# Kernel tuning notes

Measured on AMD Instinct MI355X. Metric: run time of the kernel, lower is better.

The kernel has to match this reference:

```python
import jax, jax.numpy as jnp
import numpy as np

B, T, C, H, MEM = 2, 2048, 1024, 16, 256
HD = C // H


def setup_inputs() -> dict:
    key = jax.random.key(0)
    ks = jax.random.split(key, 6)
    return {
        "x": jax.random.normal(ks[0], (B, T, C), dtype=jnp.float32),
        "ext_mem": jax.random.normal(ks[1], (B, MEM, C), dtype=jnp.float32),
        "W_attn": jax.random.normal(ks[2], (C, 3 * C), dtype=jnp.float32) * 0.02,
        "b_attn": jax.random.normal(ks[3], (3 * C,), dtype=jnp.float32) * 0.02,
        "W_proj": jax.random.normal(ks[4], (C, C), dtype=jnp.float32) * 0.02,
        "b_proj": jax.random.normal(ks[5], (C,), dtype=jnp.float32) * 0.02,
    }


def reference(x, ext_mem, W_attn, b_attn, W_proj, b_proj):
    Bx, Tx, Cx = x.shape
    qkv = x @ W_attn + b_attn                      # [B,T,3C]
    q, k, v = jnp.split(qkv, 3, axis=-1)
    # [B,H,T,HD]
    q = q.reshape(Bx, Tx, H, HD).transpose(0, 2, 1, 3)
    k = k.reshape(Bx, Tx, H, HD).transpose(0, 2, 1, 3)
    v = v.reshape(Bx, Tx, H, HD).transpose(0, 2, 1, 3)
    mem = ext_mem.reshape(Bx, -1, H, HD).transpose(0, 2, 1, 3)  # [B,H,MEM,HD]
    k = jnp.concatenate([mem, k], axis=2)          # [B,H,MEM+T,HD]
    v = jnp.concatenate([mem, v], axis=2)
    mem_len = k.shape[2] - Tx
    scale = 1.0 / jnp.sqrt(jnp.float32(HD))
    att = jnp.einsum("bhtd,bhsd->bhts", q, k) * scale  # [B,H,T,MEM+T]
    # memory prefix fully attended; causal over the T query positions
    rows = jnp.arange(Tx)[:, None]
    cols = jnp.arange(mem_len + Tx)[None, :]
    allowed = (cols < mem_len) | ((cols - mem_len) <= rows)  # [T,MEM+T]
    att = jnp.where(allowed[None, None], att, jnp.float32(-jnp.inf))
    att = jax.nn.softmax(att, axis=-1)
    y = jnp.einsum("bhts,bhsd->bhtd", att, v)      # [B,H,T,HD]
    y = y.transpose(0, 2, 1, 3).reshape(Bx, Tx, Cx)
    return y @ W_proj + b_proj
```

## Files before the change

kernel.cpp:

```cpp
#include <hip/hip_runtime.h>

#define B_    2
#define T_    2048
#define C_    1024
#define H_    16
#define HD_   64
#define MEM_  256
#define S_    2304
#define NKT_  36

typedef __attribute__((ext_vector_type(8))) short short8;
typedef __attribute__((ext_vector_type(4))) short short4v;
typedef __attribute__((ext_vector_type(4))) float f32x4;

__device__ __forceinline__ unsigned short f2bf(float x) {
    return (unsigned short)((__float_as_uint(x) + 0x8000u) >> 16);
}

__device__ __forceinline__ unsigned int pk2bf(float lo, float hi) {
    unsigned int a = __float_as_uint(lo) + 0x8000u;
    unsigned int b = __float_as_uint(hi) + 0x8000u;
    return __builtin_amdgcn_perm(b, a, 0x07060302);
}

typedef const __attribute__((address_space(1))) unsigned int* gp_t;
typedef __attribute__((address_space(3))) unsigned int* lp_t;

__device__ __forceinline__ void gll16(const unsigned short* g, unsigned short* l) {
    __builtin_amdgcn_global_load_lds((gp_t)g, (lp_t)l, 16, 0, 0);
}

#define C1_ 0.18033688011112042f

__global__ __launch_bounds__(256) void prep_all(
    const float* __restrict__ x, const float* __restrict__ Wa,
    const float* __restrict__ Wp, const float* __restrict__ ext,
    unsigned short* __restrict__ x_tl, unsigned short* __restrict__ WtA,
    unsigned short* __restrict__ WtP, unsigned short* __restrict__ k_ws,
    unsigned short* __restrict__ v_tl)
{
    __shared__ float L[64][65];
    const int bid = blockIdx.x, tid = threadIdx.x;
    if (bid < 4096) {
        int i = bid * 256 + tid;
        int c = (i & 255) * 4;
        int m = i >> 8;
        float4 v = ((const float4*)x)[i];
        ushort4 o;
        o.x = f2bf(v.x); o.y = f2bf(v.y); o.z = f2bf(v.z); o.w = f2bf(v.w);
        int mt = m >> 7, r = m & 127, kc = c >> 5, cc = c & 31;
        int p = (cc >> 3) ^ ((r >> 1) & 3);
        *(ushort4*)&x_tl[(((size_t)mt * 32 + kc) << 12) + (r << 5) + p * 8 + (cc & 7)] = o;
    } else if (bid < 5120) {
        const float* in; unsigned short* out; int Cc, r0, c0;
        if (bid < 4864) {
            int r = bid - 4096; in = Wa; out = WtA; Cc = 3 * C_;
            c0 = (r % 48) * 64; r0 = (r / 48) * 64;
        } else {
            int r = bid - 4864; in = Wp; out = WtP; Cc = C_;
            c0 = (r & 15) * 64; r0 = (r >> 4) * 64;
        }
        const int jj = tid >> 4;
        const int i4 = (tid & 15) * 4;
#pragma unroll
        for (int t = 0; t < 4; ++t) {
            int j = jj + t * 16;
            float4 v = *(const float4*)(in + (size_t)(r0 + j) * Cc + c0 + i4);
            L[i4 + 0][j] = v.x; L[i4 + 1][j] = v.y;
            L[i4 + 2][j] = v.z; L[i4 + 3][j] = v.w;
        }
        __syncthreads();
#pragma unroll
        for (int t = 0; t < 4; ++t) {
            int n = c0 + jj + t * 16;
            int k = r0 + i4;
            ushort4 o;
            o.x = f2bf(L[jj + t * 16][i4 + 0]); o.y = f2bf(L[jj + t * 16][i4 + 1]);
            o.z = f2bf(L[jj + t * 16][i4 + 2]); o.w = f2bf(L[jj + t * 16][i4 + 3]);
            int nt = n >> 7, r = n & 127, kc = k >> 5, cc = k & 31;
            int p = (cc >> 3) ^ ((r >> 1) & 3);
            *(ushort4*)&out[(((size_t)nt * 32 + kc) << 12) + (r << 5) + p * 8 + (cc & 7)] = o;
        }
    } else {
        int idx = (bid - 5120) * 256 + tid;
        float val = ext[idx];
        int c = idx & (C_ - 1), m = (idx >> 10) & (MEM_ - 1), b = idx >> 18;
        int h = c >> 6, d = c & 63;
        int bh = b * H_ + h;
        unsigned short bv = f2bf(val);
        k_ws[(size_t)bh * S_ * 64 + (size_t)m * 64 + (((d >> 3) ^ (m & 7)) << 3) + (d & 7)] = bv;
        int ts = m >> 6, key = m & 63;
        v_tl[(((size_t)bh * NKT_ + ts) * 64 + d) * 64 + (((key >> 3) ^ (d & 7)) << 3) + (key & 7)] = bv;
    }
}

__global__ __launch_bounds__(256) void qkv_gemm(
    const unsigned short* __restrict__ A,
    const unsigned short* __restrict__ Bt,
    const float* __restrict__ bias,
    unsigned short* __restrict__ q_ws,
    unsigned short* __restrict__ k_ws,
    unsigned short* __restrict__ v_tl)
{
    __shared__ __align__(16) unsigned short As[2][4096];
    __shared__ __align__(16) unsigned short Bs[2][4096];
    const int tid = threadIdx.x, lane = tid & 63, wave = tid >> 6;
    const int wr = wave >> 1, wc = wave & 1;
    const size_t abase = (size_t)blockIdx.y * 32 * 4096;
    const size_t bbase = (size_t)blockIdx.x * 32 * 4096;

    f32x4 acc[4][4];
#pragma unroll
    for (int i = 0; i < 4; ++i)
#pragma unroll
        for (int j = 0; j < 4; ++j) acc[i][j] = (f32x4){0.f, 0.f, 0.f, 0.f};

    auto stage = [&](int kc, int buf) {
        const unsigned short* ga = A + abase + (size_t)kc * 4096;
        const unsigned short* gb = Bt + bbase + (size_t)kc * 4096;
#pragma unroll
        for (int s = 0; s < 2; ++s) {
            int seg = wave + s * 4;
            gll16(ga + seg * 512 + lane * 8, &As[buf][seg * 512]);
            gll16(gb + seg * 512 + lane * 8, &Bs[buf][seg * 512]);
        }
    };

    stage(0, 0);
    __syncthreads();
    for (int kc = 0; kc < 32; ++kc) {
        if (kc + 1 < 32) stage(kc + 1, (kc + 1) & 1);
        const unsigned short* as = As[kc & 1];
        const unsigned short* bs = Bs[kc & 1];
        short8 af[4], bf4[4];
#pragma unroll
        for (int i = 0; i < 4; ++i) {
            int row = wr * 64 + i * 16 + (lane & 15);
            int ph = (lane >> 4) ^ ((row >> 1) & 3);
            af[i] = *(const short8*)&as[row * 32 + ph * 8];
        }
#pragma unroll
        for (int j = 0; j < 4; ++j) {
            int row = wc * 64 + j * 16 + (lane & 15);
            int ph = (lane >> 4) ^ ((row >> 1) & 3);
            bf4[j] = *(const short8*)&bs[row * 32 + ph * 8];
        }
#pragma unroll
        for (int i = 0; i < 4; ++i)
#pragma unroll
            for (int j = 0; j < 4; ++j)
                acc[i][j] = __builtin_amdgcn_mfma_f32_16x16x32_bf16(
                    af[i], bf4[j], acc[i][j], 0, 0, 0);
        __syncthreads();
    }

#pragma unroll
    for (int j = 0; j < 4; ++j) {
        int n = blockIdx.x * 128 + wc * 64 + j * 16 + (lane & 15);
        float bs = bias[n];
        int sel = n >> 10, h = (n >> 6) & 15, d = n & 63;
#pragma unroll
        for (int i = 0; i < 4; ++i) {
            int m = blockIdx.y * 128 + wr * 64 + i * 16 + (lane >> 4) * 4;
            int b = m >> 11, t0 = m & (T_ - 1);
            int bh = b * H_ + h;
            if (sel == 0) {
                size_t base = ((size_t)bh * T_ + t0) * 64 + d;
#pragma unroll
                for (int r = 0; r < 4; ++r)
                    q_ws[base + (size_t)r * 64] = f2bf((acc[i][j][r] + bs) * C1_);
            } else if (sel == 1) {
#pragma unroll
                for (int r = 0; r < 4; ++r) {
                    int s = MEM_ + t0 + r;
                    k_ws[(size_t)bh * S_ * 64 + (size_t)s * 64
                         + (((d >> 3) ^ (s & 7)) << 3) + (d & 7)] =
                        f2bf(acc[i][j][r] + bs);
                }
            } else {
                int s0 = MEM_ + t0, ts = s0 >> 6, key = s0 & 63;
                ushort4 pv;
                pv.x = f2bf(acc[i][j][0] + bs);
                pv.y = f2bf(acc[i][j][1] + bs);
                pv.z = f2bf(acc[i][j][2] + bs);
                pv.w = f2bf(acc[i][j][3] + bs);
                *(ushort4*)&v_tl[(((size_t)bh * NKT_ + ts) * 64 + d) * 64
                                 + (((key >> 3) ^ (d & 7)) << 3) + (key & 7)] = pv;
            }
        }
    }
}

__global__ __launch_bounds__(256) void proj_gemm(
    const unsigned short* __restrict__ A,
    const unsigned short* __restrict__ Bt,
    const float* __restrict__ bias,
    float* __restrict__ out)
{
    __shared__ __align__(16) unsigned short As[2][2048];
    __shared__ __align__(16) unsigned short Bs[2][4096];
    const int tid = threadIdx.x, lane = tid & 63, wave = tid >> 6;
    const int m64 = blockIdx.y;
    const size_t abase = ((size_t)(m64 >> 1) * 32) * 4096 + (size_t)(m64 & 1) * 2048;
    const size_t bbase = (size_t)blockIdx.x * 32 * 4096;

    f32x4 acc[4][2];
#pragma unroll
    for (int i = 0; i < 4; ++i)
#pragma unroll
        for (int j = 0; j < 2; ++j) acc[i][j] = (f32x4){0.f, 0.f, 0.f, 0.f};

    auto stage = [&](int kc, int buf) {
        const unsigned short* ga = A + abase + (size_t)kc * 4096;
        const unsigned short* gb = Bt + bbase + (size_t)kc * 4096;
        gll16(ga + wave * 512 + lane * 8, &As[buf][wave * 512]);
        gll16(gb + wave * 512 + lane * 8, &Bs[buf][wave * 512]);
        gll16(gb + (wave + 4) * 512 + lane * 8, &Bs[buf][(wave + 4) * 512]);
    };

    stage(0, 0);
    __syncthreads();
    for (int kc = 0; kc < 32; ++kc) {
        if (kc + 1 < 32) stage(kc + 1, (kc + 1) & 1);
        const unsigned short* as = As[kc & 1];
        const unsigned short* bs = Bs[kc & 1];
        short8 af[4], bf2[2];
#pragma unroll
        for (int i = 0; i < 4; ++i) {
            int row = i * 16 + (lane & 15);
            int ph = (lane >> 4) ^ ((row >> 1) & 3);
            af[i] = *(const short8*)&as[row * 32 + ph * 8];
        }
#pragma unroll
        for (int j = 0; j < 2; ++j) {
            int row = wave * 32 + j * 16 + (lane & 15);
            int ph = (lane >> 4) ^ ((row >> 1) & 3);
            bf2[j] = *(const short8*)&bs[row * 32 + ph * 8];
        }
#pragma unroll
        for (int i = 0; i < 4; ++i)
#pragma unroll
            for (int j = 0; j < 2; ++j)
                acc[i][j] = __builtin_amdgcn_mfma_f32_16x16x32_bf16(
                    af[i], bf2[j], acc[i][j], 0, 0, 0);
        __syncthreads();
    }

#pragma unroll
    for (int j = 0; j < 2; ++j) {
        int n = blockIdx.x * 128 + wave * 32 + j * 16 + (lane & 15);
        float bs = bias[n];
#pragma unroll
        for (int i = 0; i < 4; ++i) {
            int m = m64 * 64 + i * 16 + (lane >> 4) * 4;
#pragma unroll
            for (int r = 0; r < 4; ++r)
                out[(size_t)(m + r) * C_ + n] = acc[i][j][r] + bs;
        }
    }
}

__global__ __launch_bounds__(256, 4) void flash_mfma(
    const unsigned short* __restrict__ qg,
    const unsigned short* __restrict__ kg,
    const unsigned short* __restrict__ vg,
    unsigned short* __restrict__ yt)
{
    __shared__ __align__(16) unsigned short Ks[2][4096];
    __shared__ __align__(16) unsigned short Vs[2][4096];

    const int tid = threadIdx.x, lane = tid & 63, wq = tid >> 6;
    const int quad = lane >> 4;
    const int a = blockIdx.x;
    const int h = blockIdx.y, b = blockIdx.z;
    const int qt = (h & 8) ? a : (31 - a);
    const int nt = 5 + qt;
    const int bh = b * H_ + h;
    const size_t kgb = (size_t)bh * S_ * 64;
    const size_t vgb = (size_t)bh * NKT_ * 4096;

    short8 qf[2];
    {
        const unsigned short* p = qg + ((size_t)bh * T_ + qt * 64 + wq * 16
                                        + (lane & 15)) * 64 + quad * 8;
        qf[0] = *(const short8*)p; qf[1] = *(const short8*)(p + 32);
    }

    f32x4 o[4];
#pragma unroll
    for (int j = 0; j < 4; ++j) o[j] = (f32x4){0.f, 0.f, 0.f, 0.f};
    float l = 0.f;

    const unsigned short* kB0 = &Ks[0][(lane & 15) * 64 + ((quad ^ (lane & 7)) * 8)];
    const unsigned short* kB1 = &Ks[0][(lane & 15) * 64 + (((quad + 4) ^ (lane & 7)) * 8)];
    const unsigned short* vPs[4];
#pragma unroll
    for (int kb = 0; kb < 4; ++kb)
        vPs[kb] = &Vs[0][(lane & 15) * 64
                         + (((kb * 2 + (lane >> 5)) ^ (lane & 7)) * 8)
                         + (quad & 1) * 4];

    auto stageTo = [&](int kt, int ofs) {
        const unsigned short* gk = kg + kgb + (size_t)kt * 4096;
        const unsigned short* gv = vg + vgb + (size_t)kt * 4096;
        gll16(gk + wq * 512 + lane * 8, &Ks[0][ofs + wq * 512]);
        gll16(gk + (wq + 4) * 512 + lane * 8, &Ks[0][ofs + (wq + 4) * 512]);
        gll16(gv + wq * 512 + lane * 8, &Vs[0][ofs + wq * 512]);
        gll16(gv + (wq + 4) * 512 + lane * 8, &Vs[0][ofs + (wq + 4) * 512]);
    };

    const int tq = qt * 64 + wq * 16 + (lane & 15);

    stageTo(0, 0);
    stageTo(1, 4096);
    for (int kt = 0; kt < nt; ++kt) {
        const int B = (kt & 1) << 12;
        if (kt + 1 < nt) asm volatile("s_waitcnt vmcnt(4)" ::: "memory");
        else             asm volatile("s_waitcnt vmcnt(0)" ::: "memory");
        __builtin_amdgcn_s_barrier();
        __builtin_amdgcn_sched_barrier(0);
        {
            const bool diag = (kt == nt - 1);
            const int s0 = kt * 64;
            short8 kA[4][2];
#pragma unroll
            for (int kb = 0; kb < 4; ++kb) {
                kA[kb][0] = *(const short8*)&kB0[B + kb * 1024];
                kA[kb][1] = *(const short8*)&kB1[B + kb * 1024];
            }
            short4v vF[4][4];
#pragma unroll
            for (int kb = 0; kb < 4; ++kb)
#pragma unroll
                for (int dblk = 0; dblk < 4; ++dblk)
                    vF[kb][dblk] = *(const short4v*)&vPs[kb][B + dblk * 1024];

#pragma unroll
            for (int kb = 0; kb < 4; ++kb) {
                f32x4 z = (f32x4){0.f, 0.f, 0.f, 0.f};
                z = __builtin_amdgcn_mfma_f32_16x16x32_bf16(kA[kb][0], qf[0], z, 0, 0, 0);
                z = __builtin_amdgcn_mfma_f32_16x16x32_bf16(kA[kb][1], qf[1], z, 0, 0, 0);
                float p[4];
#pragma unroll
                for (int r = 0; r < 4; ++r) {
                    float e = exp2f(z[r]);
                    if (diag) {
                        int key = s0 + kb * 16 + quad * 4 + r;
                        if (key - MEM_ > tq) e = 0.f;
                    }
                    l += e;
                    p[r] = e;
                }
                unsigned int r01 = pk2bf(p[0], p[1]);
                unsigned int r23 = pk2bf(p[2], p[3]);
                short4v pf;
                *(unsigned int*)&pf = r01;
                *((unsigned int*)&pf + 1) = r23;
#pragma unroll
                for (int dblk = 0; dblk < 4; ++dblk)
                    o[dblk] = __builtin_amdgcn_mfma_f32_16x16x16bf16_1k(
                        pf, vF[kb][dblk], o[dblk], 0, 0, 0);
            }
        }
        asm volatile("s_waitcnt lgkmcnt(0)" ::: "memory");
        __builtin_amdgcn_s_barrier();
        if (kt + 2 < nt) stageTo(kt + 2, B);
    }

    l += __shfl_xor(l, 16);
    l += __shfl_xor(l, 32);
    float linv[4];
#pragma unroll
    for (int r = 0; r < 4; ++r)
        linv[r] = 1.f / __shfl(l, quad * 4 + r);
#pragma unroll
    for (int dblk = 0; dblk < 4; ++dblk) {
        int c = h * 64 + dblk * 16 + (lane & 15);
        int kc = c >> 5, cc = c & 31;
#pragma unroll
        for (int r = 0; r < 4; ++r) {
            int t = qt * 64 + wq * 16 + quad * 4 + r;
            int m = b * T_ + t;
            int mt = m >> 7, rr = m & 127;
            int p = (cc >> 3) ^ ((rr >> 1) & 3);
            yt[(((size_t)mt * 32 + kc) << 12) + (rr << 5) + p * 8 + (cc & 7)] =
                f2bf(o[dblk][r] * linv[r]);
        }
    }
}

extern "C" void kernel_launch(void* const* d_in, const int* in_sizes, int n_in,
                              void* d_out, int out_size, void* d_ws, size_t ws_size,
                              hipStream_t stream) {
    (void)in_sizes; (void)n_in; (void)out_size; (void)ws_size;
    const float* x      = (const float*)d_in[0];
    const float* ext    = (const float*)d_in[1];
    const float* W_attn = (const float*)d_in[2];
    const float* b_attn = (const float*)d_in[3];
    const float* W_proj = (const float*)d_in[4];
    const float* b_proj = (const float*)d_in[5];
    float* out = (float*)d_out;

    unsigned short* x_tl  = (unsigned short*)d_ws;
    unsigned short* WtA   = x_tl + 4194304;
    unsigned short* WtP   = WtA + 3145728;
    unsigned short* q_ws  = WtP + 1048576;
    unsigned short* k_ws  = q_ws + 4194304;
    unsigned short* v_tl  = k_ws + 4718592;
    unsigned short* y_tl  = v_tl + 4718592;

    dim3 blk(256);
    prep_all<<<7168, blk, 0, stream>>>(x, W_attn, W_proj, ext,
                                       x_tl, WtA, WtP, k_ws, v_tl);
    qkv_gemm<<<dim3(24, 32), blk, 0, stream>>>(
        x_tl, WtA, b_attn, q_ws, k_ws, v_tl);
    flash_mfma<<<dim3(32, H_, B_), blk, 0, stream>>>(q_ws, k_ws, v_tl, y_tl);
    proj_gemm<<<dim3(8, 64), blk, 0, stream>>>(y_tl, WtP, b_proj, out);
}
```

Before: 202.2 us.

## Double query tile per flash block to reuse staged K/V across two row groups

```diff
diff --git a/kernel.cpp b/kernel.cpp
--- a/kernel.cpp
+++ b/kernel.cpp
@@ -260,7 +260,7 @@
     }
 }
 
-__global__ __launch_bounds__(256, 4) void flash_mfma(
+__global__ __launch_bounds__(256, 2) void flash_mfma(
     const unsigned short* __restrict__ qg,
     const unsigned short* __restrict__ kg,
     const unsigned short* __restrict__ vg,
@@ -273,23 +273,26 @@
     const int quad = lane >> 4;
     const int a = blockIdx.x;
     const int h = blockIdx.y, b = blockIdx.z;
-    const int qt = (h & 8) ? a : (31 - a);
-    const int nt = 5 + qt;
+    const int qt = ((b ^ (h >> 3)) & 1) ? a : (15 - a);
+    const int nt = 2 * qt + 6;
     const int bh = b * H_ + h;
     const size_t kgb = (size_t)bh * S_ * 64;
     const size_t vgb = (size_t)bh * NKT_ * 4096;
 
-    short8 qf[2];
+    short8 qf[2][2];
     {
-        const unsigned short* p = qg + ((size_t)bh * T_ + qt * 64 + wq * 16
+        const unsigned short* p = qg + ((size_t)bh * T_ + qt * 128 + wq * 32
                                         + (lane & 15)) * 64 + quad * 8;
-        qf[0] = *(const short8*)p; qf[1] = *(const short8*)(p + 32);
-    }
-
-    f32x4 o[4];
-#pragma unroll
-    for (int j = 0; j < 4; ++j) o[j] = (f32x4){0.f, 0.f, 0.f, 0.f};
-    float l = 0.f;
+        qf[0][0] = *(const short8*)p;            qf[0][1] = *(const short8*)(p + 32);
+        qf[1][0] = *(const short8*)(p + 1024);   qf[1][1] = *(const short8*)(p + 1056);
+    }
+
+    f32x4 o[2][4];
+#pragma unroll
+    for (int f = 0; f < 2; ++f)
+#pragma unroll
+        for (int j = 0; j < 4; ++j) o[f][j] = (f32x4){0.f, 0.f, 0.f, 0.f};
+    float l0 = 0.f, l1 = 0.f;
 
     const unsigned short* kB0 = &Ks[0][(lane & 15) * 64 + ((quad ^ (lane & 7)) * 8)];
     const unsigned short* kB1 = &Ks[0][(lane & 15) * 64 + (((quad + 4) ^ (lane & 7)) * 8)];
@@ -309,7 +312,8 @@
         gll16(gv + (wq + 4) * 512 + lane * 8, &Vs[0][ofs + (wq + 4) * 512]);
     };
 
-    const int tq = qt * 64 + wq * 16 + (lane & 15);
+    const int tq0 = qt * 128 + wq * 32 + (lane & 15);
+    const int tq1 = tq0 + 16;
 
     stageTo(0, 0);
     stageTo(1, 4096);
@@ -319,8 +323,9 @@
         else             asm volatile("s_waitcnt vmcnt(0)" ::: "memory");
         __builtin_amdgcn_s_barrier();
         __builtin_amdgcn_sched_barrier(0);
-        {
-            const bool diag = (kt == nt - 1);
+        const bool skip = (kt * 64 - MEM_ > qt * 128 + wq * 32 + 31);
+        if (!skip) {
+            const bool diag = (kt >= nt - 2);
             const int s0 = kt * 64;
             short8 kA[4][2];
 #pragma unroll
@@ -337,29 +342,37 @@
 
 #pragma unroll
             for (int kb = 0; kb < 4; ++kb) {
-                f32x4 z = (f32x4){0.f, 0.f, 0.f, 0.f};
-                z = __builtin_amdgcn_mfma_f32_16x16x32_bf16(kA[kb][0], qf[0], z, 0, 0, 0);
-                z = __builtin_amdgcn_mfma_f32_16x16x32_bf16(kA[kb][1], qf[1], z, 0, 0, 0);
-                float p[4];
+                f32x4 z0 = (f32x4){0.f, 0.f, 0.f, 0.f};
+                f32x4 z1 = (f32x4){0.f, 0.f, 0.f, 0.f};
+                z0 = __builtin_amdgcn_mfma_f32_16x16x32_bf16(kA[kb][0], qf[0][0], z0, 0, 0, 0);
+                z0 = __builtin_amdgcn_mfma_f32_16x16x32_bf16(kA[kb][1], qf[0][1], z0, 0, 0, 0);
+                z1 = __builtin_amdgcn_mfma_f32_16x16x32_bf16(kA[kb][0], qf[1][0], z1, 0, 0, 0);
+                z1 = __builtin_amdgcn_mfma_f32_16x16x32_bf16(kA[kb][1], qf[1][1], z1, 0, 0, 0);
+                float p0[4], p1[4];
 #pragma unroll
                 for (int r = 0; r < 4; ++r) {
-                    float e = exp2f(z[r]);
+                    float e0 = exp2f(z0[r]);
+                    float e1 = exp2f(z1[r]);
                     if (diag) {
                         int key = s0 + kb * 16 + quad * 4 + r;
-                        if (key - MEM_ > tq) e = 0.f;
+                        if (key - MEM_ > tq0) e0 = 0.f;
+                        if (key - MEM_ > tq1) e1 = 0.f;
                     }
-                    l += e;
-                    p[r] = e;
+                    l0 += e0; p0[r] = e0;
+                    l1 += e1; p1[r] = e1;
                 }
-                unsigned int r01 = pk2bf(p[0], p[1]);
-                unsigned int r23 = pk2bf(p[2], p[3]);
-                short4v pf;
-                *(unsigned int*)&pf = r01;
-                *((unsigned int*)&pf + 1) = r23;
-#pragma unroll
-                for (int dblk = 0; dblk < 4; ++dblk)
-                    o[dblk] = __builtin_amdgcn_mfma_f32_16x16x16bf16_1k(
-                        pf, vF[kb][dblk], o[dblk], 0, 0, 0);
+                short4v pf0, pf1;
+                *(unsigned int*)&pf0       = pk2bf(p0[0], p0[1]);
+                *((unsigned int*)&pf0 + 1) = pk2bf(p0[2], p0[3]);
+                *(unsigned int*)&pf1       = pk2bf(p1[0], p1[1]);
+                *((unsigned int*)&pf1 + 1) = pk2bf(p1[2], p1[3]);
+#pragma unroll
+                for (int dblk = 0; dblk < 4; ++dblk) {
+                    o[0][dblk] = __builtin_amdgcn_mfma_f32_16x16x16bf16_1k(
+                        pf0, vF[kb][dblk], o[0][dblk], 0, 0, 0);
+                    o[1][dblk] = __builtin_amdgcn_mfma_f32_16x16x16bf16_1k(
+                        pf1, vF[kb][dblk], o[1][dblk], 0, 0, 0);
+                }
             }
         }
         asm volatile("s_waitcnt lgkmcnt(0)" ::: "memory");
@@ -367,24 +380,35 @@
         if (kt + 2 < nt) stageTo(kt + 2, B);
     }
 
-    l += __shfl_xor(l, 16);
-    l += __shfl_xor(l, 32);
-    float linv[4];
-#pragma unroll
-    for (int r = 0; r < 4; ++r)
-        linv[r] = 1.f / __shfl(l, quad * 4 + r);
+    l0 += __shfl_xor(l0, 16); l0 += __shfl_xor(l0, 32);
+    l1 += __shfl_xor(l1, 16); l1 += __shfl_xor(l1, 32);
+    float linv0[4], linv1[4];
+#pragma unroll
+    for (int r = 0; r < 4; ++r) {
+        linv0[r] = 1.f / __shfl(l0, quad * 4 + r);
+        linv1[r] = 1.f / __shfl(l1, quad * 4 + r);
+    }
 #pragma unroll
     for (int dblk = 0; dblk < 4; ++dblk) {
         int c = h * 64 + dblk * 16 + (lane & 15);
         int kc = c >> 5, cc = c & 31;
 #pragma unroll
         for (int r = 0; r < 4; ++r) {
-            int t = qt * 64 + wq * 16 + quad * 4 + r;
-            int m = b * T_ + t;
-            int mt = m >> 7, rr = m & 127;
-            int p = (cc >> 3) ^ ((rr >> 1) & 3);
-            yt[(((size_t)mt * 32 + kc) << 12) + (rr << 5) + p * 8 + (cc & 7)] =
-                f2bf(o[dblk][r] * linv[r]);
+            int t0 = qt * 128 + wq * 32 + quad * 4 + r;
+            {
+                int m = b * T_ + t0;
+                int mt = m >> 7, rr = m & 127;
+                int p = (cc >> 3) ^ ((rr >> 1) & 3);
+                yt[(((size_t)mt * 32 + kc) << 12) + (rr << 5) + p * 8 + (cc & 7)] =
+                    f2bf(o[0][dblk][r] * linv0[r]);
+            }
+            {
+                int m = b * T_ + t0 + 16;
+                int mt = m >> 7, rr = m & 127;
+                int p = (cc >> 3) ^ ((rr >> 1) & 3);
+                yt[(((size_t)mt * 32 + kc) << 12) + (rr << 5) + p * 8 + (cc & 7)] =
+                    f2bf(o[1][dblk][r] * linv1[r]);
+            }
         }
     }
 }
@@ -414,6 +438,6 @@
                                        x_tl, WtA, WtP, k_ws, v_tl);
     qkv_gemm<<<dim3(24, 32), blk, 0, stream>>>(
         x_tl, WtA, b_attn, q_ws, k_ws, v_tl);
-    flash_mfma<<<dim3(32, H_, B_), blk, 0, stream>>>(q_ws, k_ws, v_tl, y_tl);
+    flash_mfma<<<dim3(16, H_, B_), blk, 0, stream>>>(q_ws, k_ws, v_tl, y_tl);
     proj_gemm<<<dim3(8, 64), blk, 0, stream>>>(y_tl, WtP, b_proj, out);
 }
```

Result: slower. 213.2 us (+5.4%).
